# Optimization experiments

Hardware: AMD Instinct MI355X
Metric: run time of the kernel (lower is better)

The kernel has to match this reference:

```python
import jax, jax.numpy as jnp
import numpy as np

DIM = 512
HEADS = 8
HEAD_DIM = DIM // HEADS
B, N = 4, 8192


def setup_inputs() -> dict:
    key = jax.random.key(0)
    k1, k2, k3, k4 = jax.random.split(key, 4)
    x = jax.random.normal(k1, (B, N, DIM), dtype=jnp.float32)
    # torch Linear weight is [out, in]; store transposed [in, out] for x @ W
    Wqkv = jax.random.normal(k2, (DIM, 3 * DIM), dtype=jnp.float32) * (DIM ** -0.5)
    Wout = jax.random.normal(k3, (DIM, DIM), dtype=jnp.float32) * (DIM ** -0.5)
    bout = jax.random.normal(k4, (DIM,), dtype=jnp.float32) * 0.01
    return {"x": x, "Wqkv": Wqkv, "Wout": Wout, "bout": bout}


def reference(x, Wqkv, Wout, bout):
    b, n, d = x.shape
    h, hd = HEADS, HEAD_DIM
    qkv = x @ Wqkv  # [b, n, 3d]
    q, k, v = jnp.split(qkv, 3, axis=-1)
    # [b, n, d] -> [b, h, n, hd]
    def to_heads(t):
        return t.reshape(b, n, h, hd).transpose(0, 2, 1, 3)
    q, k, v = to_heads(q), to_heads(k), to_heads(v)
    q = jax.nn.elu(q) + 1.0
    k = jax.nn.elu(k) + 1.0
    kv = jnp.einsum('bhnd,bhne->bhde', k, v)          # [b,h,hd,hd]
    z = 1.0 / (jnp.einsum('bhnd,bhd->bhn', q, k.sum(axis=2)) + 1e-6)
    out = jnp.einsum('bhnd,bhde->bhne', q, kv) * z[..., None]
    out = out.transpose(0, 2, 1, 3).reshape(b, n, d)
    # dropout in eval mode is identity
    return out @ Wout + bout
```

## Files before the change

### kernel.cpp

```cpp
#include <hip/hip_runtime.h>

typedef unsigned short u16;
typedef __bf16 bf16x8 __attribute__((ext_vector_type(8)));
typedef float f32x4 __attribute__((ext_vector_type(4)));

#define DEV static __device__ __forceinline__

DEV float bf2f(u16 u) { unsigned x = ((unsigned)u) << 16; return __builtin_bit_cast(float, x); }
DEV u16 f2bf(float f) {
  unsigned u = __builtin_bit_cast(unsigned, f);
  u += 0x7FFFu + ((u >> 16) & 1u);
  return (u16)(u >> 16);
}

#define GLD_LDS16(gp, lp)                                                    \
  __builtin_amdgcn_global_load_lds(                                          \
      (__attribute__((address_space(1))) void*)(void*)(gp),                  \
      (__attribute__((address_space(3))) void*)(lp), 16, 0, 0)

#define BAR() __builtin_amdgcn_s_barrier()
#define WAIT_LGKM0()                                                         \
  { asm volatile("s_waitcnt lgkmcnt(0)" ::: "memory");                       \
    __builtin_amdgcn_sched_barrier(0); }
#define WAIT_VM(n) asm volatile("s_waitcnt vmcnt(" #n ")" ::: "memory")

__global__ __launch_bounds__(256) void convert_bf16_kernel(
    const float* __restrict__ in, u16* __restrict__ out) {
  const size_t i = (size_t)blockIdx.x * 256 + threadIdx.x;
  const float4* p = (const float4*)in + 2 * i;
  float4 a = p[0], b = p[1];
  unsigned w0 = (unsigned)f2bf(a.x) | ((unsigned)f2bf(a.y) << 16);
  unsigned w1 = (unsigned)f2bf(a.z) | ((unsigned)f2bf(a.w) << 16);
  unsigned w2 = (unsigned)f2bf(b.x) | ((unsigned)f2bf(b.y) << 16);
  unsigned w3 = (unsigned)f2bf(b.z) | ((unsigned)f2bf(b.w) << 16);
  ((uint4*)out)[i] = make_uint4(w0, w1, w2, w3);
}

__global__ void transpose_bf16(const float* __restrict__ W, u16* __restrict__ Wt,
                               int K, int Ncols) {
  __shared__ float t[32][33];
  const int tx = threadIdx.x & 31, ty = threadIdx.x >> 5;
  const int n0 = blockIdx.x * 32, k0 = blockIdx.y * 32;
#pragma unroll
  for (int i = 0; i < 4; ++i)
    t[ty + i * 8][tx] = W[(size_t)(k0 + ty + i * 8) * Ncols + n0 + tx];
  __syncthreads();
#pragma unroll
  for (int i = 0; i < 4; ++i)
    Wt[(size_t)(n0 + ty + i * 8) * K + k0 + tx] = f2bf(t[tx][ty + i * 8]);
}

template <int MODE>
__global__ __launch_bounds__(512, 2) void gemm8_kernel(
    const u16* __restrict__ A, const u16* __restrict__ Bt,
    u16* __restrict__ qb, u16* __restrict__ kb, u16* __restrict__ vb,
    float* __restrict__ Cf, const float* __restrict__ bias) {
  constexpr int NX = (MODE == 0) ? 6 : 2;
  constexpr int K = 512;
  __shared__ __align__(16) u16 As[2][2][8192];
  __shared__ __align__(16) u16 Bs[2][2][8192];

  const int tid = threadIdx.x;
  const int lane = tid & 63;
  const int wid = tid >> 6;
  const int wr = wid >> 2;
  const int wcn = wid & 3;

  const int nwg = gridDim.x;
  const int pb = blockIdx.x;
  const int logical = (pb & 7) * (nwg >> 3) + (pb >> 3);
  const int rowBase = (logical / NX) * 256;
  const int colBase = (logical % NX) * 256;

  int soff[2], od[2];
#pragma unroll
  for (int i = 0; i < 2; ++i) {
    int o = (wid * 2 + i) * 1024 + lane * 16;
    int a = o ^ (((o >> 7) & 7) << 4);
    soff[i] = (a >> 7) * K + ((a & 127) >> 1);
    od[i] = (wid * 2 + i) * 512;
  }
  const u16* Abase = A + (size_t)rowBase * K;
  const u16* Bbase = Bt + (size_t)colBase * K;

#define STAGE_A(tau, h)                                                      \
  { const u16* g = Abase + (size_t)(h)*128 * K + (tau)*64;                   \
    _Pragma("unroll") for (int i = 0; i < 2; ++i)                            \
        GLD_LDS16(g + soff[i], &As[(tau)&1][h][od[i]]); }
#define STAGE_B(tau, h)                                                      \
  { const u16* g = Bbase + (size_t)(h)*128 * K + (tau)*64;                   \
    _Pragma("unroll") for (int i = 0; i < 2; ++i)                            \
        GLD_LDS16(g + soff[i], &Bs[(tau)&1][h][od[i]]); }

  const int sx = (lane & 7) << 4;
  int rb[2];
#pragma unroll
  for (int ks = 0; ks < 2; ++ks)
    rb[ks] = ((lane & 15) * 128 + ks * 64 + (lane >> 4) * 16) ^ sx;
  const char* Ahalf[2] = {(const char*)&As[0][wr][0], (const char*)&As[1][wr][0]};
  const char* Bhalf[2] = {(const char*)&Bs[0][wcn >> 1][0], (const char*)&Bs[1][wcn >> 1][0]};

  bf16x8 aA[4][2], bB0[2][2], bB1[2][2];
  f32x4 acc[8][4];
  f32x4 zv = {0.f, 0.f, 0.f, 0.f};
#pragma unroll
  for (int m = 0; m < 8; ++m)
#pragma unroll
    for (int n = 0; n < 4; ++n) acc[m][n] = zv;

#define LDA_FRAGS(par, mh)                                                   \
  _Pragma("unroll") for (int m = 0; m < 4; ++m)                              \
      _Pragma("unroll") for (int ks = 0; ks < 2; ++ks)                       \
          aA[m][ks] = *(const bf16x8*)(Ahalf[par] + (mh)*8192 + m * 2048 + rb[ks]);
#define LDB_FRAGS(par, nh, dst)                                              \
  _Pragma("unroll") for (int n = 0; n < 2; ++n)                              \
      _Pragma("unroll") for (int ks = 0; ks < 2; ++ks)                       \
          dst[n][ks] = *(const bf16x8*)(Bhalf[par] + (wcn & 1) * 8192 +      \
                                        (nh)*4096 + n * 2048 + rb[ks]);
#define MFMA_QUAD(mh, nh, bsrc)                                              \
  __builtin_amdgcn_s_setprio(1);                                             \
  _Pragma("unroll") for (int m = 0; m < 4; ++m)                              \
      _Pragma("unroll") for (int n = 0; n < 2; ++n)                          \
          _Pragma("unroll") for (int ks = 0; ks < 2; ++ks)                   \
              acc[(mh)*4 + m][(nh)*2 + n] =                                  \
                  __builtin_amdgcn_mfma_f32_16x16x32_bf16(                   \
                      aA[m][ks], bsrc[n][ks], acc[(mh)*4 + m][(nh)*2 + n],   \
                      0, 0, 0);                                              \
  __builtin_amdgcn_s_setprio(0);

  STAGE_A(0, 0); STAGE_A(0, 1); STAGE_B(0, 0); STAGE_B(0, 1);
  STAGE_B(1, 0); STAGE_A(1, 0);
  WAIT_VM(4);
  BAR();

  for (int t = 0; t < 6; t += 2) {
    LDA_FRAGS(0, 0); LDB_FRAGS(0, 0, bB0);
    STAGE_B(t + 1, 1);
    BAR(); WAIT_LGKM0();
    MFMA_QUAD(0, 0, bB0);
    BAR();
    LDB_FRAGS(0, 1, bB1);
    STAGE_A(t + 1, 1);
    BAR(); WAIT_LGKM0();
    MFMA_QUAD(0, 1, bB1);
    BAR();
    LDA_FRAGS(0, 1);
    STAGE_B(t + 2, 0);
    BAR(); WAIT_LGKM0();
    MFMA_QUAD(1, 1, bB1);
    BAR();
    STAGE_A(t + 2, 0);
    BAR(); WAIT_LGKM0();
    MFMA_QUAD(1, 0, bB0);
    WAIT_VM(4);
    BAR();
    LDA_FRAGS(1, 0); LDB_FRAGS(1, 0, bB0);
    STAGE_A(t + 2, 1);
    BAR(); WAIT_LGKM0();
    MFMA_QUAD(0, 0, bB0);
    BAR();
    LDB_FRAGS(1, 1, bB1);
    STAGE_B(t + 2, 1);
    BAR(); WAIT_LGKM0();
    MFMA_QUAD(0, 1, bB1);
    BAR();
    LDA_FRAGS(1, 1);
    STAGE_B(t + 3, 0);
    BAR(); WAIT_LGKM0();
    MFMA_QUAD(1, 1, bB1);
    BAR();
    STAGE_A(t + 3, 0);
    BAR(); WAIT_LGKM0();
    MFMA_QUAD(1, 0, bB0);
    WAIT_VM(4);
    BAR();
  }

  LDA_FRAGS(0, 0); LDB_FRAGS(0, 0, bB0);
  STAGE_B(7, 1);
  BAR(); WAIT_LGKM0();
  MFMA_QUAD(0, 0, bB0);
  BAR();
  LDB_FRAGS(0, 1, bB1);
  STAGE_A(7, 1);
  BAR(); WAIT_LGKM0();
  MFMA_QUAD(0, 1, bB1);
  BAR();
  LDA_FRAGS(0, 1);
  BAR(); WAIT_LGKM0();
  MFMA_QUAD(1, 1, bB1);
  BAR();
  BAR(); WAIT_LGKM0();
  MFMA_QUAD(1, 0, bB0);
  WAIT_VM(0);
  BAR();
  LDA_FRAGS(1, 0); LDB_FRAGS(1, 0, bB0);
  BAR(); WAIT_LGKM0();
  MFMA_QUAD(0, 0, bB0);
  BAR();
  LDB_FRAGS(1, 1, bB1);
  BAR(); WAIT_LGKM0();
  MFMA_QUAD(0, 1, bB1);
  BAR();
  LDA_FRAGS(1, 1);
  BAR(); WAIT_LGKM0();
  MFMA_QUAD(1, 1, bB1);
  BAR();
  BAR(); WAIT_LGKM0();
  MFMA_QUAD(1, 0, bB0);

  if (MODE == 0) {
    u16* dst = (colBase < 512) ? qb : (colBase < 1024) ? kb : vb;
    const int cb2 = (colBase < 512) ? colBase : (colBase < 1024) ? colBase - 512 : colBase - 1024;
    const bool doelu = (colBase < 1024);
#pragma unroll
    for (int mi = 0; mi < 8; ++mi) {
#pragma unroll
      for (int ni = 0; ni < 4; ++ni) {
        const int col = cb2 + wcn * 64 + ni * 16 + (lane & 15);
#pragma unroll
        for (int r = 0; r < 4; ++r) {
          const int row = rowBase + wr * 128 + mi * 16 + (lane >> 4) * 4 + r;
          float v = acc[mi][ni][r];
          if (doelu) v = (v > 0.f) ? v + 1.f : __expf(v);
          dst[(size_t)row * 512 + col] = f2bf(v);
        }
      }
    }
  } else {
#pragma unroll
    for (int mi = 0; mi < 8; ++mi) {
#pragma unroll
      for (int ni = 0; ni < 4; ++ni) {
        const int col = colBase + wcn * 64 + ni * 16 + (lane & 15);
#pragma unroll
        for (int r = 0; r < 4; ++r) {
          const int row = rowBase + wr * 128 + mi * 16 + (lane >> 4) * 4 + r;
          Cf[(size_t)row * 512 + col] = acc[mi][ni][r] + bias[col];
        }
      }
    }
  }
#undef STAGE_A
#undef STAGE_B
#undef LDA_FRAGS
#undef LDB_FRAGS
#undef MFMA_QUAD
}

__global__ __launch_bounds__(256, 2) void kv_partial_kernel(
    const u16* __restrict__ kb, const u16* __restrict__ vb,
    float* __restrict__ part) {
  __shared__ float kf[128][64];
  __shared__ float vf[128][64];
  const int tid = threadIdx.x;
  const int chunk = blockIdx.x;
  const int bh = blockIdx.y;
  const int b = bh >> 3, h = bh & 7;
  const size_t rbase = (size_t)b * 8192;
  const int hc = h * 64;
  const int dg = tid >> 4, eg = tid & 15;

  float acc[4][4] = {};
  float ks[4] = {};

  for (int st = 0; st < 4; ++st) {
    const int n0 = chunk * 512 + st * 128;
#pragma unroll
    for (int it = 0; it < 4; ++it) {
      int idx8 = it * 256 + tid;
      int r = idx8 >> 3, c = (idx8 & 7) * 8;
      uint4 kraw = *(const uint4*)(kb + (rbase + n0 + r) * 512 + hc + c);
      uint4 vraw = *(const uint4*)(vb + (rbase + n0 + r) * 512 + hc + c);
      unsigned kw[4] = {kraw.x, kraw.y, kraw.z, kraw.w};
      unsigned vw[4] = {vraw.x, vraw.y, vraw.z, vraw.w};
#pragma unroll
      for (int j = 0; j < 4; ++j) {
        kf[r][c + 2 * j] = bf2f((u16)(kw[j] & 0xFFFF));
        kf[r][c + 2 * j + 1] = bf2f((u16)(kw[j] >> 16));
        vf[r][c + 2 * j] = bf2f((u16)(vw[j] & 0xFFFF));
        vf[r][c + 2 * j + 1] = bf2f((u16)(vw[j] >> 16));
      }
    }
    __syncthreads();
#pragma unroll 4
    for (int n = 0; n < 128; ++n) {
      float4 kk = *(const float4*)&kf[n][dg * 4];
      float4 vv = *(const float4*)&vf[n][eg * 4];
      float ka[4] = {kk.x, kk.y, kk.z, kk.w};
      float va[4] = {vv.x, vv.y, vv.z, vv.w};
#pragma unroll
      for (int i = 0; i < 4; ++i)
#pragma unroll
        for (int j = 0; j < 4; ++j) acc[i][j] += ka[i] * va[j];
      if (eg == 0) {
#pragma unroll
        for (int i = 0; i < 4; ++i) ks[i] += ka[i];
      }
    }
    __syncthreads();
  }

  float* pp = part + ((size_t)bh * 16 + chunk) * (64 * 80);
#pragma unroll
  for (int i = 0; i < 4; ++i) {
#pragma unroll
    for (int j = 0; j < 4; ++j) pp[(dg * 4 + i) * 80 + eg * 4 + j] = acc[i][j];
    if (eg == 0) pp[(dg * 4 + i) * 80 + 64] = ks[i];
  }
}

__global__ void kv_reduce_kernel(const float* __restrict__ part,
                                 float* __restrict__ kv_ext) {
  const int idx = blockIdx.x * 256 + threadIdx.x;
  const int bh = idx / 5120;
  const int de = idx % 5120;
  const int e = de % 80;
  float s = 0.f;
  if (e <= 64) {
    for (int c = 0; c < 16; ++c) s += part[((size_t)bh * 16 + c) * 5120 + de];
  }
  kv_ext[idx] = s;
}

__global__ __launch_bounds__(256, 2) void attn_kernel(
    const u16* __restrict__ qb, const float* __restrict__ kv_ext,
    u16* __restrict__ attn) {
  __shared__ __align__(16) float kvs[64 * 80];
  __shared__ __align__(16) u16 qs[4][64 * 64];
  const int tid = threadIdx.x, lane = tid & 63, wid = tid >> 6;
  const int nchunk = blockIdx.x, bh = blockIdx.y;
  const int b = bh >> 3, h = bh & 7;

#pragma unroll
  for (int i = 0; i < 20; ++i)
    kvs[i * 256 + tid] = kv_ext[(size_t)bh * 5120 + i * 256 + tid];
  __syncthreads();

  bf16x8 bfr[5][2];
#pragma unroll
  for (int eb = 0; eb < 5; ++eb)
#pragma unroll
    for (int ksi = 0; ksi < 2; ++ksi) {
      unsigned pw[4];
#pragma unroll
      for (int jj = 0; jj < 4; ++jj) {
        int d0 = ksi * 32 + (lane >> 4) * 8 + 2 * jj;
        int e = eb * 16 + (lane & 15);
        unsigned lo = f2bf(kvs[d0 * 80 + e]);
        unsigned hi = f2bf(kvs[(d0 + 1) * 80 + e]);
        pw[jj] = lo | (hi << 16);
      }
      uint4 u = make_uint4(pw[0], pw[1], pw[2], pw[3]);
      bfr[eb][ksi] = __builtin_bit_cast(bf16x8, u);
    }

  const size_t row0 = (size_t)b * 8192 + (size_t)nchunk * 256 + wid * 64;
#pragma unroll
  for (int it = 0; it < 8; ++it) {
    int idx8 = it * 64 + lane;
    int r = idx8 >> 3, c = (idx8 & 7) * 8;
    GLD_LDS16(qb + (row0 + r) * 512 + h * 64 + c, &qs[wid][it * 512]);
  }
  asm volatile("s_waitcnt vmcnt(0)" ::: "memory");

  f32x4 zv = {0.f, 0.f, 0.f, 0.f};
  f32x4 acc[4][5];
#pragma unroll
  for (int m = 0; m < 4; ++m)
#pragma unroll
    for (int eb = 0; eb < 5; ++eb) acc[m][eb] = zv;

#pragma unroll
  for (int m = 0; m < 4; ++m)
#pragma unroll
    for (int ksi = 0; ksi < 2; ++ksi) {
      bf16x8 af = *(const bf16x8*)&qs[wid][(m * 16 + (lane & 15)) * 64 + ksi * 32 + (lane >> 4) * 8];
#pragma unroll
      for (int eb = 0; eb < 5; ++eb)
        acc[m][eb] = __builtin_amdgcn_mfma_f32_16x16x32_bf16(af, bfr[eb][ksi], acc[m][eb], 0, 0, 0);
    }

#pragma unroll
  for (int m = 0; m < 4; ++m) {
    float zr[4];
#pragma unroll
    for (int r = 0; r < 4; ++r) {
      float den = __shfl(acc[m][4][r], lane & ~15, 64);
      zr[r] = 1.f / (den + 1e-6f);
    }
#pragma unroll
    for (int eb = 0; eb < 4; ++eb)
#pragma unroll
      for (int r = 0; r < 4; ++r) {
        size_t row = row0 + m * 16 + (lane >> 4) * 4 + r;
        int col = h * 64 + eb * 16 + (lane & 15);
        attn[row * 512 + col] = f2bf(acc[m][eb][r] * zr[r]);
      }
  }
}

extern "C" void kernel_launch(void* const* d_in, const int* in_sizes, int n_in,
                              void* d_out, int out_size, void* d_ws, size_t ws_size,
                              hipStream_t stream) {
  const float* x = (const float*)d_in[0];
  const float* Wqkv = (const float*)d_in[1];
  const float* Wout = (const float*)d_in[2];
  const float* bout = (const float*)d_in[3];
  float* out = (float*)d_out;

  char* ws = (char*)d_ws;
  u16* qb = (u16*)ws;        ws += (size_t)32768 * 512 * 2;
  u16* kb = (u16*)ws;        ws += (size_t)32768 * 512 * 2;
  u16* vb = (u16*)ws;        ws += (size_t)32768 * 512 * 2;
  u16* wqkv_t = (u16*)ws;    ws += (size_t)1536 * 512 * 2;
  u16* wout_t = (u16*)ws;    ws += (size_t)512 * 512 * 2;
  float* kv_ext = (float*)ws; ws += (size_t)32 * 64 * 80 * 4;
  float* part = (float*)ws;   ws += (size_t)32 * 16 * 64 * 80 * 4;

  u16* xb = (u16*)d_out;

  convert_bf16_kernel<<<8192, 256, 0, stream>>>(x, xb);
  transpose_bf16<<<dim3(1536 / 32, 512 / 32), 256, 0, stream>>>(Wqkv, wqkv_t, 512, 1536);
  transpose_bf16<<<dim3(512 / 32, 512 / 32), 256, 0, stream>>>(Wout, wout_t, 512, 512);
  gemm8_kernel<0><<<768, 512, 0, stream>>>(xb, wqkv_t, qb, kb, vb, nullptr, nullptr);
  kv_partial_kernel<<<dim3(16, 32), 256, 0, stream>>>(kb, vb, part);
  kv_reduce_kernel<<<640, 256, 0, stream>>>(part, kv_ext);
  attn_kernel<<<dim3(32, 32), 256, 0, stream>>>(qb, kv_ext, vb);
  gemm8_kernel<1><<<256, 512, 0, stream>>>(vb, wout_t, nullptr, nullptr, nullptr, out, bout);
}
```

Before: 169.5 us.

## Store q/k/v in MFMA-fragment tiled layout and stage attention output through swizzled LDS

The QKV GEMM epilogue now writes q, k and v in a 16x16 fragment-tiled layout, so each lane stores 8-byte packed chunks instead of scattered 2-byte stores. The kv-partial and attention kernels read this tiled layout and unpack it into LDS, and the attention kernel now uses a XOR-swizzled LDS tile for Q. The attention output is also staged in LDS so it can be written to global memory as coalesced 16-byte stores. This is meant to cut uncoalesced global stores, at the cost of more unpacking arithmetic and dropping the direct global-to-LDS load path.

After: 170.0 us. About the same (+0.3%).

```diff
diff --git a/kernel.cpp b/kernel.cpp
--- a/kernel.cpp
+++ b/kernel.cpp
@@ -12,6 +12,7 @@
   u += 0x7FFFu + ((u >> 16) & 1u);
   return (u16)(u >> 16);
 }
+DEV int swz(int b) { return b ^ ((((b >> 7) & 7)) << 4); }
 
 #define GLD_LDS16(gp, lp)                                                    \
   __builtin_amdgcn_global_load_lds(                                          \
@@ -211,20 +212,24 @@
 
   if (MODE == 0) {
     u16* dst = (colBase < 512) ? qb : (colBase < 1024) ? kb : vb;
-    const int cb2 = (colBase < 512) ? colBase : (colBase < 1024) ? colBase - 512 : colBase - 1024;
+    const int cb2 = colBase & 511;
     const bool doelu = (colBase < 1024);
+    const int rbBase = (rowBase >> 4) + wr * 8;
+    const int cbBase = (cb2 >> 4) + wcn * 4;
 #pragma unroll
     for (int mi = 0; mi < 8; ++mi) {
 #pragma unroll
       for (int ni = 0; ni < 4; ++ni) {
-        const int col = cb2 + wcn * 64 + ni * 16 + (lane & 15);
+        float v[4];
 #pragma unroll
         for (int r = 0; r < 4; ++r) {
-          const int row = rowBase + wr * 128 + mi * 16 + (lane >> 4) * 4 + r;
-          float v = acc[mi][ni][r];
-          if (doelu) v = (v > 0.f) ? v + 1.f : __expf(v);
-          dst[(size_t)row * 512 + col] = f2bf(v);
+          float t2 = acc[mi][ni][r];
+          v[r] = doelu ? ((t2 > 0.f) ? t2 + 1.f : __expf(t2)) : t2;
         }
+        unsigned lo = (unsigned)f2bf(v[0]) | ((unsigned)f2bf(v[1]) << 16);
+        unsigned hi = (unsigned)f2bf(v[2]) | ((unsigned)f2bf(v[3]) << 16);
+        size_t base = (((size_t)(rbBase + mi) * 32 + (cbBase + ni)) * 64 + lane) * 4;
+        *(uint2*)(dst + base) = make_uint2(lo, hi);
       }
     }
   } else {
@@ -258,7 +263,7 @@
   const int bh = blockIdx.y;
   const int b = bh >> 3, h = bh & 7;
   const size_t rbase = (size_t)b * 8192;
-  const int hc = h * 64;
+  const int hcb = h * 4;
   const int dg = tid >> 4, eg = tid & 15;
 
   float acc[4][4] = {};
@@ -266,21 +271,26 @@
 
   for (int st = 0; st < 4; ++st) {
     const int n0 = chunk * 512 + st * 128;
+    const int rbT = (int)((rbase + n0) >> 4);
 #pragma unroll
     for (int it = 0; it < 4; ++it) {
-      int idx8 = it * 256 + tid;
-      int r = idx8 >> 3, c = (idx8 & 7) * 8;
-      uint4 kraw = *(const uint4*)(kb + (rbase + n0 + r) * 512 + hc + c);
-      uint4 vraw = *(const uint4*)(vb + (rbase + n0 + r) * 512 + hc + c);
-      unsigned kw[4] = {kraw.x, kraw.y, kraw.z, kraw.w};
-      unsigned vw[4] = {vraw.x, vraw.y, vraw.z, vraw.w};
-#pragma unroll
-      for (int j = 0; j < 4; ++j) {
-        kf[r][c + 2 * j] = bf2f((u16)(kw[j] & 0xFFFF));
-        kf[r][c + 2 * j + 1] = bf2f((u16)(kw[j] >> 16));
-        vf[r][c + 2 * j] = bf2f((u16)(vw[j] & 0xFFFF));
-        vf[r][c + 2 * j + 1] = bf2f((u16)(vw[j] >> 16));
-      }
+      int flat = it * 256 + tid;
+      int frag = flat >> 5, w = flat & 31;
+      int rb_i = frag >> 2, cb_i = frag & 3;
+      size_t src = (((size_t)(rbT + rb_i) * 32 + hcb + cb_i) * 64 + w * 2) * 4;
+      uint4 kraw = *(const uint4*)(kb + src);
+      uint4 vraw = *(const uint4*)(vb + src);
+      int l0 = w * 2;
+      int row0 = rb_i * 16 + ((l0 >> 4) << 2);
+      int col0 = cb_i * 16 + (l0 & 15);
+      *(float2*)&kf[row0 + 0][col0] = make_float2(bf2f((u16)(kraw.x & 0xFFFF)), bf2f((u16)(kraw.z & 0xFFFF)));
+      *(float2*)&kf[row0 + 1][col0] = make_float2(bf2f((u16)(kraw.x >> 16)), bf2f((u16)(kraw.z >> 16)));
+      *(float2*)&kf[row0 + 2][col0] = make_float2(bf2f((u16)(kraw.y & 0xFFFF)), bf2f((u16)(kraw.w & 0xFFFF)));
+      *(float2*)&kf[row0 + 3][col0] = make_float2(bf2f((u16)(kraw.y >> 16)), bf2f((u16)(kraw.w >> 16)));
+      *(float2*)&vf[row0 + 0][col0] = make_float2(bf2f((u16)(vraw.x & 0xFFFF)), bf2f((u16)(vraw.z & 0xFFFF)));
+      *(float2*)&vf[row0 + 1][col0] = make_float2(bf2f((u16)(vraw.x >> 16)), bf2f((u16)(vraw.z >> 16)));
+      *(float2*)&vf[row0 + 2][col0] = make_float2(bf2f((u16)(vraw.y & 0xFFFF)), bf2f((u16)(vraw.w & 0xFFFF)));
+      *(float2*)&vf[row0 + 3][col0] = make_float2(bf2f((u16)(vraw.y >> 16)), bf2f((u16)(vraw.w >> 16)));
     }
     __syncthreads();
 #pragma unroll 4
@@ -356,13 +366,26 @@
     }
 
   const size_t row0 = (size_t)b * 8192 + (size_t)nchunk * 256 + wid * 64;
+  const int rbQ = (int)(row0 >> 4);
+  const int hcbQ = h * 4;
+  char* qsw = (char*)&qs[wid][0];
 #pragma unroll
   for (int it = 0; it < 8; ++it) {
-    int idx8 = it * 64 + lane;
-    int r = idx8 >> 3, c = (idx8 & 7) * 8;
-    GLD_LDS16(qb + (row0 + r) * 512 + h * 64 + c, &qs[wid][it * 512]);
-  }
-  asm volatile("s_waitcnt vmcnt(0)" ::: "memory");
+    int flat = it * 64 + lane;
+    int frag = flat >> 5, w = flat & 31;
+    int rb_i = frag >> 2, cb_i = frag & 3;
+    size_t src = (((size_t)(rbQ + rb_i) * 32 + hcbQ + cb_i) * 64 + w * 2) * 4;
+    uint4 q4 = *(const uint4*)(qb + src);
+    int l0 = w * 2;
+    int row = rb_i * 16 + ((l0 >> 4) << 2);
+    int col = cb_i * 16 + (l0 & 15);
+    int bb = row * 128 + col * 2;
+    *(unsigned*)(qsw + swz(bb)) = (q4.x & 0xFFFF) | ((q4.z & 0xFFFF) << 16);
+    *(unsigned*)(qsw + swz(bb + 128)) = (q4.x >> 16) | (q4.z & 0xFFFF0000u);
+    *(unsigned*)(qsw + swz(bb + 256)) = (q4.y & 0xFFFF) | ((q4.w & 0xFFFF) << 16);
+    *(unsigned*)(qsw + swz(bb + 384)) = (q4.y >> 16) | (q4.w & 0xFFFF0000u);
+  }
+  WAIT_LGKM0();
 
   f32x4 zv = {0.f, 0.f, 0.f, 0.f};
   f32x4 acc[4][5];
@@ -375,7 +398,8 @@
   for (int m = 0; m < 4; ++m)
 #pragma unroll
     for (int ksi = 0; ksi < 2; ++ksi) {
-      bf16x8 af = *(const bf16x8*)&qs[wid][(m * 16 + (lane & 15)) * 64 + ksi * 32 + (lane >> 4) * 8];
+      int bb = (m * 16 + (lane & 15)) * 128 + (ksi * 32 + (lane >> 4) * 8) * 2;
+      bf16x8 af = *(const bf16x8*)(qsw + swz(bb));
 #pragma unroll
       for (int eb = 0; eb < 5; ++eb)
         acc[m][eb] = __builtin_amdgcn_mfma_f32_16x16x32_bf16(af, bfr[eb][ksi], acc[m][eb], 0, 0, 0);
@@ -383,20 +407,25 @@
 
 #pragma unroll
   for (int m = 0; m < 4; ++m) {
-    float zr[4];
 #pragma unroll
     for (int r = 0; r < 4; ++r) {
       float den = __shfl(acc[m][4][r], lane & ~15, 64);
-      zr[r] = 1.f / (den + 1e-6f);
-    }
-#pragma unroll
-    for (int eb = 0; eb < 4; ++eb)
-#pragma unroll
-      for (int r = 0; r < 4; ++r) {
-        size_t row = row0 + m * 16 + (lane >> 4) * 4 + r;
-        int col = h * 64 + eb * 16 + (lane & 15);
-        attn[row * 512 + col] = f2bf(acc[m][eb][r] * zr[r]);
+      float zr = 1.f / (den + 1e-6f);
+      int row = m * 16 + (lane >> 4) * 4 + r;
+#pragma unroll
+      for (int eb = 0; eb < 4; ++eb) {
+        int col = eb * 16 + (lane & 15);
+        *(u16*)(qsw + swz(row * 128 + col * 2)) = f2bf(acc[m][eb][r] * zr);
       }
+    }
+  }
+  WAIT_LGKM0();
+#pragma unroll
+  for (int jt = 0; jt < 8; ++jt) {
+    int flat = jt * 64 + lane;
+    int row = flat >> 3, w = flat & 7;
+    uint4 val = *(const uint4*)(qsw + swz(row * 128 + w * 16));
+    *(uint4*)(attn + (row0 + row) * 512 + h * 64 + w * 8) = val;
   }
 }
 
```
